# Optimization experiments

Measured on AMD Instinct MI355X. Metric: run time of the kernel, lower is better.

The kernel has to match this reference:

```python
import jax, jax.numpy as jnp
import numpy as np

H = 8       # n_heads
N = 128     # n_vars
HEAD = 64   # per-head dim (== __init__ dim)


def setup_inputs() -> dict:
    key = jax.random.key(0)
    k0, k1, k2, k3, k4 = jax.random.split(key, 5)
    B, L = 4, 8192
    D = H * HEAD
    x = jax.random.normal(k0, (B, L, D), dtype=jnp.float32)
    # nn.Linear default init: U(-1/sqrt(fan_in), 1/sqrt(fan_in)), fan_in = HEAD
    s = 1.0 / np.sqrt(HEAD)
    w1 = jax.random.uniform(k1, (HEAD, HEAD), jnp.float32, -s, s)
    b1 = jax.random.uniform(k2, (HEAD,), jnp.float32, -s, s)
    w2 = jax.random.uniform(k3, (HEAD, HEAD), jnp.float32, -s, s)
    b2 = jax.random.uniform(k4, (HEAD,), jnp.float32, -s, s)
    return {"x": x, "w1": w1, "b1": b1, "w2": w2, "b2": b2}


def reference(x, w1, b1, w2, b2):
    B, L, D = x.shape
    P = L // N  # patches per variable
    # (B,L,D) -> (B,H,L,HEAD) -> (B,H,N,P,HEAD)
    xh = x.reshape(B, L, H, HEAD).transpose(0, 2, 1, 3).reshape(B, H, N, P, HEAD)
    q = xh @ w1.T + b1  # proj_1
    k = xh @ w2.T + b2  # proj_2
    # per (b,h,patch) NxN adjacency over variables
    adj = jax.nn.gelu(jnp.einsum('bhixd,bhjxd->bhxij', q, k), approximate=False)
    adj = jax.nn.softmax(adj, axis=-1)
    # dropout is identity in eval mode; F.normalize(p=1): divide by max(L1, eps)
    adj = adj / jnp.maximum(jnp.sum(jnp.abs(adj), axis=-1, keepdims=True), 1e-12)
    out = jnp.einsum('bhxij,bhjxd->bixhd', adj, xh)  # (B,N,P,H,HEAD)
    return out.reshape(B, L, H * HEAD)
```

## Files before the change

### kernel.cpp

```cpp
#include <hip/hip_runtime.h>
#include <math.h>


namespace {
constexpr int H = 8, NV = 128, HEAD = 64, B = 4, L = 8192;
constexpr int P = L / NV;
constexpr int D = H * HEAD;
constexpr int RS = P * D;

constexpr int XT_S = 136;
constexpr int TA_S = 72;

typedef _Float16 half8  __attribute__((ext_vector_type(8)));
typedef _Float16 half2v __attribute__((ext_vector_type(2)));
typedef __fp16   fp16x2 __attribute__((ext_vector_type(2)));
typedef float    floatx4 __attribute__((ext_vector_type(4)));

__device__ __forceinline__ floatx4 mfma16(half8 a, half8 b, floatx4 c) {
    return __builtin_amdgcn_mfma_f32_16x16x32_f16(a, b, c, 0, 0, 0);
}

__device__ __forceinline__ half8 cvt8(float4 a, float4 b) {
    fp16x2 p0 = __builtin_amdgcn_cvt_pkrtz(a.x, a.y);
    fp16x2 p1 = __builtin_amdgcn_cvt_pkrtz(a.z, a.w);
    fp16x2 p2 = __builtin_amdgcn_cvt_pkrtz(b.x, b.y);
    fp16x2 p3 = __builtin_amdgcn_cvt_pkrtz(b.z, b.w);
    half8 r;
    r[0] = (_Float16)p0[0]; r[1] = (_Float16)p0[1];
    r[2] = (_Float16)p1[0]; r[3] = (_Float16)p1[1];
    r[4] = (_Float16)p2[0]; r[5] = (_Float16)p2[1];
    r[6] = (_Float16)p3[0]; r[7] = (_Float16)p3[1];
    return r;
}

__global__ __launch_bounds__(256) void pack_g(
    const float* __restrict__ w1, const float* __restrict__ w2,
    const float* __restrict__ b1, const float* __restrict__ b2,
    _Float16* __restrict__ gth, float* __restrict__ g1f,
    float* __restrict__ g2f, float* __restrict__ cf)
{
    const int t = threadIdx.x;
    if (blockIdx.x == 16) {
        if (t < 64) {
            float a = 0.f;
            #pragma unroll 8
            for (int n = 0; n < 64; ++n) a = fmaf(w1[n * 64 + t], b2[n], a);
            g1f[t] = a;
        } else if (t < 128) {
            const int d = t - 64;
            float a = 0.f;
            #pragma unroll 8
            for (int n = 0; n < 64; ++n) a = fmaf(w2[n * 64 + d], b1[n], a);
            g2f[d] = a;
        } else if (t == 128) {
            float a = 0.f;
            for (int n = 0; n < 64; ++n) a = fmaf(b1[n], b2[n], a);
            cf[0] = a;
        }
        return;
    }
    const int gid = blockIdx.x * 256 + t;
    const int d = gid & 63, e = gid >> 6;
    float a = 0.f;
    #pragma unroll 8
    for (int n = 0; n < 64; ++n) a = fmaf(w1[n * 64 + d], w2[n * 64 + e], a);
    gth[e * 64 + d] = (_Float16)a;
}

__global__ __launch_bounds__(256, 4) void space_graph_mfma4(
    const float* __restrict__ x, const _Float16* __restrict__ gth,
    const float* __restrict__ g1f, const float* __restrict__ g2f,
    const float* __restrict__ cf, float* __restrict__ out)
{
    __shared__ _Float16 lds[64 * XT_S + NV * TA_S];
    __shared__ float uv[2 * NV];
    _Float16* Xt = lds;
    _Float16* TA = lds + 64 * XT_S;
    float* u_lds = uv;
    float* v_lds = uv + NV;

    const int t    = threadIdx.x;
    const int lane = t & 63;
    const int w    = t >> 6;
    const int col  = lane & 15;
    const int quad = lane >> 4;

    const int blk = blockIdx.x;
    const int p = blk & (P - 1);
    const int h = (blk >> 6) & (H - 1);
    const int b = blk >> 9;
    const size_t base = ((size_t)b * L + (size_t)p) * D + (size_t)h * HEAD;

    {
        const int c  = t & 15;
        const int tt = t >> 4;
        #pragma unroll
        for (int it = 0; it < 4; ++it) {
            const int j0 = 2 * (tt + 16 * it);
            const float4 v0 = *(const float4*)(x + base + (size_t)j0 * RS + c * 4);
            const float4 v1 = *(const float4*)(x + base + (size_t)(j0 + 1) * RS + c * 4);
            const float va[4] = {v0.x, v0.y, v0.z, v0.w};
            const float vb[4] = {v1.x, v1.y, v1.z, v1.w};
            #pragma unroll
            for (int q = 0; q < 4; ++q) {
                half2v pr; pr[0] = (_Float16)va[q]; pr[1] = (_Float16)vb[q];
                *(half2v*)&Xt[(4 * c + q) * XT_S + j0] = pr;
            }
        }
    }

    floatx4 tacc[2][4];
    #pragma unroll
    for (int mt = 0; mt < 2; ++mt)
        #pragma unroll
        for (int nt = 0; nt < 4; ++nt) tacc[mt][nt] = (floatx4)0.0f;

    half8 axf[2][2];
    float up[2] = {0.f, 0.f}, vp[2] = {0.f, 0.f};
    #pragma unroll
    for (int ks = 0; ks < 2; ++ks) {
        const float4 ga = *(const float4*)(g1f + quad * 8 + 32 * ks);
        const float4 gb = *(const float4*)(g1f + quad * 8 + 32 * ks + 4);
        const float4 ha = *(const float4*)(g2f + quad * 8 + 32 * ks);
        const float4 hb = *(const float4*)(g2f + quad * 8 + 32 * ks + 4);
        #pragma unroll
        for (int mt = 0; mt < 2; ++mt) {
            const int row = 32 * w + 16 * mt + col;
            const float* src = x + base + (size_t)row * RS + quad * 8 + 32 * ks;
            const float4 v0 = *(const float4*)src;
            const float4 v1 = *(const float4*)(src + 4);
            axf[mt][ks] = cvt8(v0, v1);
            up[mt] += v0.x * ga.x + v0.y * ga.y + v0.z * ga.z + v0.w * ga.w
                    + v1.x * gb.x + v1.y * gb.y + v1.z * gb.z + v1.w * gb.w;
            vp[mt] += v0.x * ha.x + v0.y * ha.y + v0.z * ha.z + v0.w * ha.w
                    + v1.x * hb.x + v1.y * hb.y + v1.z * hb.z + v1.w * hb.w;
        }
    }

    #pragma unroll
    for (int ks = 0; ks < 2; ++ks)
        #pragma unroll
        for (int nt = 0; nt < 4; ++nt) {
            const half8 gb8 = *(const half8*)&gth[(col + 16 * nt) * HEAD + quad * 8 + 32 * ks];
            #pragma unroll
            for (int mt = 0; mt < 2; ++mt)
                tacc[mt][nt] = mfma16(axf[mt][ks], gb8, tacc[mt][nt]);
        }

    #pragma unroll
    for (int mt = 0; mt < 2; ++mt) {
        float uu = up[mt]; uu += __shfl_xor(uu, 16); uu += __shfl_xor(uu, 32);
        float vv = vp[mt]; vv += __shfl_xor(vv, 16); vv += __shfl_xor(vv, 32);
        if (quad == 0) u_lds[32 * w + 16 * mt + col] = uu;
        if (quad == 1) v_lds[32 * w + 16 * mt + col] = vv;
    }

    #pragma unroll
    for (int mt = 0; mt < 2; ++mt)
        #pragma unroll
        for (int r = 0; r < 4; ++r) {
            const int R = 32 * w + 16 * mt + quad * 4 + r;
            _Float16* trow = &TA[R * TA_S + col];
            #pragma unroll
            for (int nt = 0; nt < 4; ++nt)
                trow[nt * 16] = (_Float16)(tacc[mt][nt][r]);
        }
    __syncthreads();

    const float cc = cf[0];
    float ucr[2][4];
    #pragma unroll
    for (int mt = 0; mt < 2; ++mt)
        #pragma unroll
        for (int r = 0; r < 4; ++r)
            ucr[mt][r] = u_lds[32 * w + 16 * mt + quad * 4 + r] + cc;
    float vrow[8];
    #pragma unroll
    for (int nt = 0; nt < 8; ++nt) vrow[nt] = v_lds[col + 16 * nt];

    floatx4 sacc[2][8];
    #pragma unroll
    for (int mt = 0; mt < 2; ++mt)
        #pragma unroll
        for (int nt = 0; nt < 8; ++nt)
            #pragma unroll
            for (int r = 0; r < 4; ++r)
                sacc[mt][nt][r] = ucr[mt][r] + vrow[nt];

    #pragma unroll
    for (int ks = 0; ks < 2; ++ks) {
        half8 taf[2];
        #pragma unroll
        for (int mt = 0; mt < 2; ++mt)
            taf[mt] = *(const half8*)&TA[(32 * w + 16 * mt + col) * TA_S + quad * 8 + 32 * ks];
        #pragma unroll
        for (int nt = 0; nt < 8; ++nt) {
            const float* bs = x + base + (size_t)(col + 16 * nt) * RS + quad * 8 + 32 * ks;
            const half8 xb = cvt8(*(const float4*)bs, *(const float4*)(bs + 4));
            #pragma unroll
            for (int mt = 0; mt < 2; ++mt)
                sacc[mt][nt] = mfma16(taf[mt], xb, sacc[mt][nt]);
        }
    }

    #pragma unroll
    for (int mt = 0; mt < 2; ++mt)
        #pragma unroll
        for (int r = 0; r < 4; ++r) {
            float wv[8]; float rs = 0.f;
            #pragma unroll
            for (int nt = 0; nt < 8; ++nt) {
                const float s  = sacc[mt][nt][r];
                const float u  = s * fmaf(s * s, 0.035677408137f, 0.7978845608f);
                const float em = __expf(-2.0f * u);
                const float g  = s * __builtin_amdgcn_rcpf(1.0f + em);
                const float e  = __expf(g);
                wv[nt] = e; rs += e;
            }
            rs += __shfl_xor(rs, 1); rs += __shfl_xor(rs, 2);
            rs += __shfl_xor(rs, 4); rs += __shfl_xor(rs, 8);
            const float inv = __builtin_amdgcn_rcpf(rs);
            #pragma unroll
            for (int nt = 0; nt < 8; ++nt) sacc[mt][nt][r] = wv[nt] * inv;
        }

    #pragma unroll
    for (int mt = 0; mt < 2; ++mt)
        #pragma unroll
        for (int r = 0; r < 4; ++r) {
            const int R = 32 * w + 16 * mt + quad * 4 + r;
            _Float16* arow = &TA[R * TA_S + col];
            #pragma unroll
            for (int nt = 0; nt < 4; ++nt)
                arow[nt * 16] = (_Float16)(sacc[mt][nt][r]);
        }

    floatx4 oacc[2][4];
    #pragma unroll
    for (int mt = 0; mt < 2; ++mt)
        #pragma unroll
        for (int nt = 0; nt < 4; ++nt) oacc[mt][nt] = (floatx4)0.0f;

    #pragma unroll
    for (int kh = 0; kh < 2; ++kh) {
        half8 aaf[2];
        #pragma unroll
        for (int mt = 0; mt < 2; ++mt)
            aaf[mt] = *(const half8*)&TA[(32 * w + 16 * mt + col) * TA_S + quad * 8 + 32 * kh];
        #pragma unroll
        for (int nt = 0; nt < 4; ++nt) {
            const half8 xb = *(const half8*)&Xt[(col + 16 * nt) * XT_S + quad * 8 + 32 * kh];
            #pragma unroll
            for (int mt = 0; mt < 2; ++mt)
                oacc[mt][nt] = mfma16(aaf[mt], xb, oacc[mt][nt]);
        }
    }

    #pragma unroll
    for (int mt = 0; mt < 2; ++mt)
        #pragma unroll
        for (int r = 0; r < 4; ++r) {
            const int R = 32 * w + 16 * mt + quad * 4 + r;
            _Float16* arow = &TA[R * TA_S + col];
            #pragma unroll
            for (int nt = 4; nt < 8; ++nt)
                arow[(nt - 4) * 16] = (_Float16)(sacc[mt][nt][r]);
        }

    #pragma unroll
    for (int kh = 0; kh < 2; ++kh) {
        half8 aaf[2];
        #pragma unroll
        for (int mt = 0; mt < 2; ++mt)
            aaf[mt] = *(const half8*)&TA[(32 * w + 16 * mt + col) * TA_S + quad * 8 + 32 * kh];
        #pragma unroll
        for (int nt = 0; nt < 4; ++nt) {
            const half8 xb = *(const half8*)&Xt[(col + 16 * nt) * XT_S + quad * 8 + 32 * (kh + 2)];
            #pragma unroll
            for (int mt = 0; mt < 2; ++mt)
                oacc[mt][nt] = mfma16(aaf[mt], xb, oacc[mt][nt]);
        }
    }

    #pragma unroll
    for (int mt = 0; mt < 2; ++mt)
        #pragma unroll
        for (int r = 0; r < 4; ++r) {
            const int i = 32 * w + 16 * mt + quad * 4 + r;
            float* orow = out + base + (size_t)i * RS + col;
            #pragma unroll
            for (int nt = 0; nt < 4; ++nt)
                orow[nt * 16] = oacc[mt][nt][r];
        }
}
}

extern "C" void kernel_launch(void* const* d_in, const int* in_sizes, int n_in,
                              void* d_out, int out_size, void* d_ws, size_t ws_size,
                              hipStream_t stream) {
    const float* x  = (const float*)d_in[0];
    const float* w1 = (const float*)d_in[1];
    const float* b1 = (const float*)d_in[2];
    const float* w2 = (const float*)d_in[3];
    const float* b2 = (const float*)d_in[4];
    float* out = (float*)d_out;

    _Float16* gth = (_Float16*)d_ws;
    float* g1f = (float*)((char*)d_ws + 8192);
    float* g2f = g1f + 64;
    float* cf  = g2f + 64;

    hipLaunchKernelGGL(pack_g, dim3(17), dim3(256), 0, stream,
                       w1, w2, b1, b2, gth, g1f, g2f, cf);
    hipLaunchKernelGGL(space_graph_mfma4, dim3(B * H * P), dim3(256), 0, stream,
                       x, gth, g1f, g2f, cf, out);
}
```

Baseline: 170.1 us.

## Stage row-major fp16 X tile in LDS instead of re-reading global x for scores

Adds a row-major fp16 copy of the 128x64 X tile to LDS, written during the initial load, so the score MFMA B-operands come from LDS instead of being re-fetched from global memory and converted. The u values now move via lane shuffles, and the v values are stored in the padding columns of the transposed tile, which removes the separate uv array. The extra LDS lowers the occupancy hint from 4 to 3 blocks per CU, so latency hiding may get worse.

```diff
diff --git a/kernel.cpp b/kernel.cpp
--- a/kernel.cpp
+++ b/kernel.cpp
@@ -9,9 +9,11 @@
 constexpr int RS = P * D;
 
 constexpr int XT_S = 136;
+constexpr int XH_S = 72;
 constexpr int TA_S = 72;
 
 typedef _Float16 half8  __attribute__((ext_vector_type(8)));
+typedef _Float16 half4h __attribute__((ext_vector_type(4)));
 typedef _Float16 half2v __attribute__((ext_vector_type(2)));
 typedef __fp16   fp16x2 __attribute__((ext_vector_type(2)));
 typedef float    floatx4 __attribute__((ext_vector_type(4)));
@@ -31,6 +33,10 @@
     r[4] = (_Float16)p2[0]; r[5] = (_Float16)p2[1];
     r[6] = (_Float16)p3[0]; r[7] = (_Float16)p3[1];
     return r;
+}
+
+__device__ __forceinline__ float& vslot(_Float16* xt, int j) {
+    return ((float*)(xt + (size_t)(j >> 2) * XT_S + 128))[j & 3];
 }
 
 __global__ __launch_bounds__(256) void pack_g(
@@ -67,17 +73,15 @@
     gth[e * 64 + d] = (_Float16)a;
 }
 
-__global__ __launch_bounds__(256, 4) void space_graph_mfma4(
+__global__ __launch_bounds__(256, 3) void space_graph_mfma5(
     const float* __restrict__ x, const _Float16* __restrict__ gth,
     const float* __restrict__ g1f, const float* __restrict__ g2f,
     const float* __restrict__ cf, float* __restrict__ out)
 {
-    __shared__ _Float16 lds[64 * XT_S + NV * TA_S];
-    __shared__ float uv[2 * NV];
+    __shared__ _Float16 lds[64 * XT_S + NV * XH_S + NV * TA_S];
     _Float16* Xt = lds;
-    _Float16* TA = lds + 64 * XT_S;
-    float* u_lds = uv;
-    float* v_lds = uv + NV;
+    _Float16* Xh = lds + 64 * XT_S;
+    _Float16* TA = Xh + NV * XH_S;
 
     const int t    = threadIdx.x;
     const int lane = t & 63;
@@ -101,11 +105,17 @@
             const float4 v1 = *(const float4*)(x + base + (size_t)(j0 + 1) * RS + c * 4);
             const float va[4] = {v0.x, v0.y, v0.z, v0.w};
             const float vb[4] = {v1.x, v1.y, v1.z, v1.w};
+            half4h ra, rb;
             #pragma unroll
             for (int q = 0; q < 4; ++q) {
-                half2v pr; pr[0] = (_Float16)va[q]; pr[1] = (_Float16)vb[q];
+                const _Float16 ha = (_Float16)va[q];
+                const _Float16 hb = (_Float16)vb[q];
+                ra[q] = ha; rb[q] = hb;
+                half2v pr; pr[0] = ha; pr[1] = hb;
                 *(half2v*)&Xt[(4 * c + q) * XT_S + j0] = pr;
             }
+            *(half4h*)&Xh[(size_t)j0 * XH_S + 4 * c] = ra;
+            *(half4h*)&Xh[(size_t)(j0 + 1) * XH_S + 4 * c] = rb;
         }
     }
 
@@ -147,12 +157,13 @@
                 tacc[mt][nt] = mfma16(axf[mt][ks], gb8, tacc[mt][nt]);
         }
 
+    float ureg[2];
     #pragma unroll
     for (int mt = 0; mt < 2; ++mt) {
         float uu = up[mt]; uu += __shfl_xor(uu, 16); uu += __shfl_xor(uu, 32);
         float vv = vp[mt]; vv += __shfl_xor(vv, 16); vv += __shfl_xor(vv, 32);
-        if (quad == 0) u_lds[32 * w + 16 * mt + col] = uu;
-        if (quad == 1) v_lds[32 * w + 16 * mt + col] = vv;
+        ureg[mt] = uu;
+        if (quad == 0) vslot(Xt, 32 * w + 16 * mt + col) = vv;
     }
 
     #pragma unroll
@@ -173,10 +184,10 @@
     for (int mt = 0; mt < 2; ++mt)
         #pragma unroll
         for (int r = 0; r < 4; ++r)
-            ucr[mt][r] = u_lds[32 * w + 16 * mt + quad * 4 + r] + cc;
+            ucr[mt][r] = __shfl(ureg[mt], quad * 4 + r) + cc;
     float vrow[8];
     #pragma unroll
-    for (int nt = 0; nt < 8; ++nt) vrow[nt] = v_lds[col + 16 * nt];
+    for (int nt = 0; nt < 8; ++nt) vrow[nt] = vslot(Xt, col + 16 * nt);
 
     floatx4 sacc[2][8];
     #pragma unroll
@@ -195,8 +206,7 @@
             taf[mt] = *(const half8*)&TA[(32 * w + 16 * mt + col) * TA_S + quad * 8 + 32 * ks];
         #pragma unroll
         for (int nt = 0; nt < 8; ++nt) {
-            const float* bs = x + base + (size_t)(col + 16 * nt) * RS + quad * 8 + 32 * ks;
-            const half8 xb = cvt8(*(const float4*)bs, *(const float4*)(bs + 4));
+            const half8 xb = *(const half8*)&Xh[(col + 16 * nt) * XH_S + quad * 8 + 32 * ks];
             #pragma unroll
             for (int mt = 0; mt < 2; ++mt)
                 sacc[mt][nt] = mfma16(taf[mt], xb, sacc[mt][nt]);
@@ -312,6 +322,6 @@
 
     hipLaunchKernelGGL(pack_g, dim3(17), dim3(256), 0, stream,
                        w1, w2, b1, b2, gth, g1f, g2f, cf);
-    hipLaunchKernelGGL(space_graph_mfma4, dim3(B * H * P), dim3(256), 0, stream,
+    hipLaunchKernelGGL(space_graph_mfma5, dim3(B * H * P), dim3(256), 0, stream,
                        x, gth, g1f, g2f, cf, out);
 }
```

Result: faster. 142.3 us (-16.4%).
